# Performance work log

Measured on AMD Instinct MI355X. Metric: run time of the kernel, lower is better.

The kernel has to match this reference:

```python
import jax, jax.numpy as jnp
import numpy as np

B, F, V, D, K = 16384, 39, 30000, 16, 20
EPS = 1e-5


def bn_eval(x, g, b):
    # inference-mode BatchNorm1d with running_mean=0, running_var=1
    return g * x / jnp.sqrt(1.0 + EPS) + b


def setup_inputs() -> dict:
    key = jax.random.key(0)
    ks = jax.random.split(key, 12)
    x = jax.random.randint(ks[0], (B, F), 0, V)
    emb_table = jax.random.normal(ks[1], (F * V, D), dtype=jnp.float32) * 0.05
    w_c = jax.random.normal(ks[2], (F, F * D), dtype=jnp.float32) * 0.05
    w0 = jax.random.normal(ks[3], (1024, F * D), dtype=jnp.float32) * 0.04
    w1 = jax.random.normal(ks[4], (512, 1024), dtype=jnp.float32) * 0.03
    w_out = jax.random.normal(ks[5], (1, 512), dtype=jnp.float32) * 0.04
    return {
        'x': x, 'emb_table': emb_table,
        'w_c': w_c, 'b_c': jnp.zeros((F,)), 'g_c': jnp.ones((F,)), 'be_c': jnp.zeros((F,)),
        'w0': w0, 'b0': jnp.zeros((1024,)), 'g0': jnp.ones((1024,)), 'be0': jnp.zeros((1024,)),
        'w1': w1, 'b1': jnp.zeros((512,)), 'g1': jnp.ones((512,)), 'be1': jnp.zeros((512,)),
        'w_out': w_out, 'b_out': jnp.zeros((1,)),
    }


def reference(x, emb_table, w_c, b_c, g_c, be_c, w0, b0, g0, be0,
              w1, b1, g1, be1, w_out, b_out):
    offsets = jnp.arange(F, dtype=x.dtype) * V          # per-field offsets
    idx = x + offsets[None, :]                          # [B, F]
    emb = emb_table[idx]                                # [B, F, D] gather

    # controller_mlp: flatten (batch, D, F) layout like torch transpose(1,2)
    flat = jnp.transpose(emb, (0, 2, 1)).reshape(B, F * D)
    h = jax.nn.relu(bn_eval(flat @ w_c.T + b_c, g_c, be_c))
    scores = jax.nn.softmax(h, axis=1)                  # [B, F]

    # kmax_pooling: top-k field indices, sorted ascending, gather weights
    _, kidx = jax.lax.top_k(scores, K)
    kidx = jnp.sort(kidx, axis=1)                       # [B, K]
    w = jnp.take_along_axis(scores, kidx, axis=1)       # [B, K]

    # forward_select: gather selected field embeddings, weight them
    sel = jnp.take_along_axis(emb, kidx[:, :, None], axis=1)  # [B, K, D]
    weighted = sel * w[:, :, None]

    # scatter back into full field slots (unselected fields are zero)
    full = jnp.zeros((B, F, D), weighted.dtype)
    bidx = jnp.arange(B)[:, None]
    full = full.at[bidx, kidx].set(weighted)            # [B, F, D]

    z = jnp.transpose(full, (0, 2, 1)).reshape(B, F * D)
    z = jax.nn.relu(bn_eval(z @ w0.T + b0, g0, be0))
    z = jax.nn.relu(bn_eval(z @ w1.T + b1, g1, be1))
    out = jax.nn.sigmoid(z @ w_out.T + b_out)           # [B, 1]
    return out.squeeze(-1)
```

## Files before the change

### kernel.cpp

```cpp
#include <hip/hip_runtime.h>
#include <math.h>

#define B_SZ 16384
#define F_N 39
#define V_N 30000
#define D_N 16
#define K_SEL 20
#define FD 624
#define KP0 640
#define NCP 48
#define N0 1024
#define N1 512
#define CBR 16
#define ALD 648

typedef unsigned short u16;
typedef __attribute__((ext_vector_type(8))) short bf16x8;
typedef __attribute__((ext_vector_type(8))) unsigned short u16x8;
typedef __attribute__((ext_vector_type(4))) float f32x4;
typedef __attribute__((ext_vector_type(4))) unsigned short u16x4;

__device__ __forceinline__ u16 f2bf(float v) {
    union { float f; unsigned u; } x; x.f = v;
    unsigned r = x.u + 0x7fff + ((x.u >> 16) & 1);
    return (u16)(r >> 16);
}
__device__ __forceinline__ float bf2f(u16 v) {
    union { unsigned u; float f; } x; x.u = ((unsigned)v) << 16;
    return x.f;
}
__device__ __forceinline__ unsigned cvtpk2(float a, float b) {
    unsigned d;
    asm("v_cvt_pk_bf16_f32 %0, %1, %2" : "=v"(d) : "v"(a), "v"(b));
    return d;
}

#define GLD16(gp, lp) __builtin_amdgcn_global_load_lds( \
    (const __attribute__((address_space(1))) unsigned int*)(gp), \
    (__attribute__((address_space(3))) unsigned int*)(lp), 16, 0, 0)

__global__ __launch_bounds__(256) void prep_all_kernel(
    const float* __restrict__ w0, const float* __restrict__ w1,
    const float* __restrict__ w_c, const float* __restrict__ b_c,
    const float* __restrict__ g_c, const float* __restrict__ be_c,
    u16* __restrict__ w0b, u16* __restrict__ w1b, u16* __restrict__ wcb,
    float* __restrict__ bcp, float* __restrict__ gcp, float* __restrict__ becp,
    float* __restrict__ outp)
{
    __shared__ float Lb[8][624];
    const int bid = blockIdx.x;
    const int t   = threadIdx.x;

    if (bid < 134) {
        const bool is_w0 = (bid < 128);
        const int r0 = is_w0 ? bid * 8 : (bid - 128) * 8;
        const int nrows_src = is_w0 ? N0 : F_N;
        const float* __restrict__ src = is_w0 ? w0 : w_c;
        u16* __restrict__ dst = is_w0 ? w0b : wcb;

        for (int j = t; j < 8 * 156; j += 256) {
            const int row = j / 156;
            const int c4  = j - row * 156;
            const int n   = r0 + row;
            if (n < nrows_src)
                *(float4*)&Lb[row][c4 * 4] =
                    *(const float4*)&src[(size_t)n * FD + c4 * 4];
        }
        __syncthreads();

        for (int j = t; j < 8 * 320; j += 256) {
            const int row = j / 320;
            const int pr  = j - row * 320;
            const int n   = r0 + row;
            const int k0  = pr * 2;
            float v0 = 0.f, v1 = 0.f;
            if (n < nrows_src) {
                const int d0 = k0 & 15,       f0 = k0 >> 4;
                const int d1 = (k0 + 1) & 15, f1 = (k0 + 1) >> 4;
                if (f0 < F_N) v0 = Lb[row][d0 * F_N + f0];
                if (f1 < F_N) v1 = Lb[row][d1 * F_N + f1];
            }
            *(unsigned*)&dst[(size_t)n * KP0 + k0] = cvtpk2(v0, v1);
        }
        return;
    }
    if (bid < 390) {
        const size_t e0 = (size_t)(bid - 134) * 2048 + t * 8;
        float4 v0 = *(const float4*)(w1 + e0);
        float4 v1 = *(const float4*)(w1 + e0 + 4);
        uint4 o = { cvtpk2(v0.x, v0.y), cvtpk2(v0.z, v0.w),
                    cvtpk2(v1.x, v1.y), cvtpk2(v1.z, v1.w) };
        *(uint4*)(w1b + e0) = o;
        return;
    }
    if (bid < 398) {
        const size_t e0 = (size_t)(bid - 390) * 2048 + t * 8;
        float4 z = {0.f, 0.f, 0.f, 0.f};
        *(float4*)(outp + e0)     = z;
        *(float4*)(outp + e0 + 4) = z;
        return;
    }
    if (t < 3 * NCP) {
        const int which = t / NCP, n = t - which * NCP;
        float v = 0.f;
        if (n < F_N) v = (which == 0) ? b_c[n] : (which == 1) ? g_c[n] : be_c[n];
        ((which == 0) ? bcp : (which == 1) ? gcp : becp)[n] = v;
    }
}

__global__ __launch_bounds__(256) void fused_controller_kernel(
    const int* __restrict__ x, const float* __restrict__ emb_table,
    const u16* __restrict__ wcb, const float* __restrict__ bcp,
    const float* __restrict__ gcp, const float* __restrict__ becp,
    u16* __restrict__ zb)
{
    __shared__ __align__(16) u16 Al[CBR * ALD];
    __shared__ float vv[CBR][49];
    __shared__ f32x4 part[4][64][3];
    __shared__ float selw[CBR][F_N];

    const int t    = threadIdx.x;
    const int wave = t >> 6;
    const int lane = t & 63;
    const int b0   = blockIdx.x * CBR;

    {
        const int p0 = t, p1 = t + 256, p2 = t + 512;
        const int xi0 = x[b0 * F_N + p0];
        const int xi1 = x[b0 * F_N + p1];
        const int xi2 = (p2 < CBR * F_N) ? x[b0 * F_N + p2] : 0;
        const int pp[3] = { p0, p1, p2 };
        const int xx[3] = { xi0, xi1, xi2 };
        #pragma unroll
        for (int s = 0; s < 3; ++s) {
            const int p = pp[s];
            if (p < CBR * F_N) {
                const int row = p / F_N;
                const int f   = p - row * F_N;
                const float4* src =
                    (const float4*)(emb_table + (size_t)(xx[s] + f * V_N) * D_N);
                float4 v0 = src[0], v1 = src[1], v2 = src[2], v3 = src[3];
                uint4 o0 = { cvtpk2(v0.x, v0.y), cvtpk2(v0.z, v0.w),
                             cvtpk2(v1.x, v1.y), cvtpk2(v1.z, v1.w) };
                uint4 o1 = { cvtpk2(v2.x, v2.y), cvtpk2(v2.z, v2.w),
                             cvtpk2(v3.x, v3.y), cvtpk2(v3.z, v3.w) };
                *(uint4*)&Al[row * ALD + f * D_N]     = o0;
                *(uint4*)&Al[row * ALD + f * D_N + 8] = o1;
            }
        }
    }
    __syncthreads();

    const int m = lane & 15;
    const int q = lane >> 4;
    f32x4 acc0 = {}, acc1 = {}, acc2 = {};
    {
        const u16* ap  = &Al[m * ALD + wave * 160 + q * 8];
        const u16* bp0 = wcb + (size_t)(0  + m) * KP0 + wave * 160 + q * 8;
        const u16* bp1 = wcb + (size_t)(16 + m) * KP0 + wave * 160 + q * 8;
        const u16* bp2 = wcb + (size_t)(32 + m) * KP0 + wave * 160 + q * 8;
        #pragma unroll
        for (int k = 0; k < 5; ++k) {
            bf16x8 af = *(const bf16x8*)ap;
            bf16x8 b0 = *(const bf16x8*)bp0;
            bf16x8 b1 = *(const bf16x8*)bp1;
            bf16x8 b2 = *(const bf16x8*)bp2;
            acc0 = __builtin_amdgcn_mfma_f32_16x16x32_bf16(af, b0, acc0, 0, 0, 0);
            acc1 = __builtin_amdgcn_mfma_f32_16x16x32_bf16(af, b1, acc1, 0, 0, 0);
            acc2 = __builtin_amdgcn_mfma_f32_16x16x32_bf16(af, b2, acc2, 0, 0, 0);
            ap += 32; bp0 += 32; bp1 += 32; bp2 += 32;
        }
    }
    part[wave][lane][0] = acc0;
    part[wave][lane][1] = acc1;
    part[wave][lane][2] = acc2;
    __syncthreads();

    {
        f32x4 r0 = part[0][lane][0] + part[1][lane][0] + part[2][lane][0] + part[3][lane][0];
        f32x4 r1 = part[0][lane][1] + part[1][lane][1] + part[2][lane][1] + part[3][lane][1];
        f32x4 r2 = part[0][lane][2] + part[1][lane][2] + part[2][lane][2] + part[3][lane][2];

        const float rs = rsqrtf(1.0f + 1e-5f);
        if (q == wave) {
            #pragma unroll
            for (int j = 0; j < 3; ++j) {
                const f32x4 a = (j == 0) ? r0 : (j == 1) ? r1 : r2;
                const int n = j * 16 + m;
                const float gn = gcp[n] * rs;
                const float bn = becp[n];
                const float bi = bcp[n];
                #pragma unroll
                for (int r = 0; r < 4; ++r)
                    vv[wave * 4 + r][n] = fmaxf(fmaf(gn, a[r] + bi, bn), 0.f);
            }
        }
    }
    __syncthreads();

    {
        const int row = wave * 4 + (lane >> 4);
        const int fl  = lane & 15;
        float e[3] = {0.f, 0.f, 0.f};
        float mloc = -1e30f;
        #pragma unroll
        for (int it = 0; it < 3; ++it) {
            const int f = fl + 16 * it;
            if (f < F_N) { e[it] = vv[row][f]; mloc = fmaxf(mloc, e[it]); }
        }
        mloc = fmaxf(mloc, __shfl_xor(mloc, 1, 64));
        mloc = fmaxf(mloc, __shfl_xor(mloc, 2, 64));
        mloc = fmaxf(mloc, __shfl_xor(mloc, 4, 64));
        mloc = fmaxf(mloc, __shfl_xor(mloc, 8, 64));
        float sloc = 0.f;
        #pragma unroll
        for (int it = 0; it < 3; ++it) {
            const int f = fl + 16 * it;
            if (f < F_N) { e[it] = expf(e[it] - mloc); sloc += e[it]; }
        }
        sloc += __shfl_xor(sloc, 1, 64);
        sloc += __shfl_xor(sloc, 2, 64);
        sloc += __shfl_xor(sloc, 4, 64);
        sloc += __shfl_xor(sloc, 8, 64);
        const float inv = 1.f / sloc;
        #pragma unroll
        for (int it = 0; it < 3; ++it) {
            const int f = fl + 16 * it;
            if (f < F_N) vv[row][f] = e[it];
        }

        int rank[3] = {};
        for (int gg = 0; gg < F_N; ++gg) {
            const float o = vv[row][gg];
            #pragma unroll
            for (int it = 0; it < 3; ++it) {
                const int f = fl + 16 * it;
                if (f < F_N)
                    rank[it] += (o > e[it] || (o == e[it] && gg < f)) ? 1 : 0;
            }
        }
        #pragma unroll
        for (int it = 0; it < 3; ++it) {
            const int f = fl + 16 * it;
            if (f < F_N)
                selw[row][f] = (rank[it] < K_SEL) ? e[it] * inv : 0.f;
        }
    }
    __syncthreads();

    for (int gp = t; gp < CBR * 40; gp += 256) {
        const int row  = gp / 40;
        const int slot = gp - row * 40;
        u16* dst = zb + (size_t)(b0 + row) * KP0 + slot * D_N;
        uint4 o0 = {0u,0u,0u,0u}, o1 = {0u,0u,0u,0u};
        if (slot < F_N) {
            const float w = selw[row][slot];
            u16x8 a0 = *(u16x8*)&Al[row * ALD + slot * D_N];
            u16x8 a1 = *(u16x8*)&Al[row * ALD + slot * D_N + 8];
            o0 = (uint4){ cvtpk2(bf2f(a0[0]) * w, bf2f(a0[1]) * w),
                          cvtpk2(bf2f(a0[2]) * w, bf2f(a0[3]) * w),
                          cvtpk2(bf2f(a0[4]) * w, bf2f(a0[5]) * w),
                          cvtpk2(bf2f(a0[6]) * w, bf2f(a0[7]) * w) };
            o1 = (uint4){ cvtpk2(bf2f(a1[0]) * w, bf2f(a1[1]) * w),
                          cvtpk2(bf2f(a1[2]) * w, bf2f(a1[3]) * w),
                          cvtpk2(bf2f(a1[4]) * w, bf2f(a1[5]) * w),
                          cvtpk2(bf2f(a1[6]) * w, bf2f(a1[7]) * w) };
        }
        *(uint4*)dst       = o0;
        *(uint4*)(dst + 8) = o1;
    }
}

template<int MODE>
__global__ __launch_bounds__(512) void gemm_mfma_bn_relu(
    const u16* __restrict__ A, const u16* __restrict__ W,
    const float* __restrict__ bias, const float* __restrict__ g,
    const float* __restrict__ be, u16* __restrict__ Cout,
    int M, int N, int Kp,
    const float* __restrict__ w_out, float* __restrict__ outp)
{
    __shared__ __align__(16) u16 SM[3 * 12288];

    const int t    = threadIdx.x;
    const int wave = t >> 6;
    const int lane = t & 63;
    const int wm   = wave >> 1, wn = wave & 1;
    const int m0   = blockIdx.x * 256;
    const int n0   = blockIdx.y * 128;

    const int rA0 = t >> 2;
    const int cA0 = (t & 3) ^ ((rA0 >> 1) & 3);
    const int rA1 = 128 + rA0;
    const int cA1 = (t & 3) ^ ((rA1 >> 1) & 3);
    const u16* gA0 = A + (size_t)(m0 + rA0) * Kp + cA0 * 8;
    const u16* gA1 = A + (size_t)(m0 + rA1) * Kp + cA1 * 8;
    const u16* gB  = W + (size_t)(n0 + rA0) * Kp + cA0 * 8;
    const int dA0 = t * 8, dA1 = 4096 + t * 8, dB = 8192 + t * 8;

    const int q    = lane >> 4;
    const int lr16 = lane & 15;

    int aoff[4], boff[4];
    #pragma unroll
    for (int i = 0; i < 4; ++i) {
        int ra = wm * 64 + i * 16 + lr16;
        aoff[i] = ra * 32 + ((q ^ ((ra >> 1) & 3)) * 8);
        int rb = wn * 64 + i * 16 + lr16;
        boff[i] = rb * 32 + ((q ^ ((rb >> 1) & 3)) * 8);
    }

    const int NIT = Kp >> 5;

    GLD16(gA0, SM + dA0);
    GLD16(gA1, SM + dA1);
    GLD16(gB,  SM + dB);
    gA0 += 32; gA1 += 32; gB += 32;
    GLD16(gA0, SM + 12288 + dA0);
    GLD16(gA1, SM + 12288 + dA1);
    GLD16(gB,  SM + 12288 + dB);
    gA0 += 32; gA1 += 32; gB += 32;

    f32x4 acc[4][4] = {};
    int cur = 0, stg = 2;

    for (int it = 0; it < NIT - 1; ++it) {
        asm volatile("s_waitcnt vmcnt(3)" ::: "memory");
        __builtin_amdgcn_s_barrier();
        __builtin_amdgcn_sched_barrier(0);

        const u16* ac = SM + cur * 12288;
        const u16* bc = ac + 8192;

        bf16x8 af0 = *(const bf16x8*)(ac + aoff[0]);
        bf16x8 af1 = *(const bf16x8*)(ac + aoff[1]);
        bf16x8 b0v = *(const bf16x8*)(bc + boff[0]);
        bf16x8 b1v = *(const bf16x8*)(bc + boff[1]);
        bf16x8 b2v = *(const bf16x8*)(bc + boff[2]);
        bf16x8 b3v = *(const bf16x8*)(bc + boff[3]);

        if (it + 2 < NIT) {
            u16* s = SM + stg * 12288;
            GLD16(gA0, s + dA0);
            GLD16(gA1, s + dA1);
            GLD16(gB,  s + dB);
            gA0 += 32; gA1 += 32; gB += 32;
        }

        asm volatile("s_waitcnt lgkmcnt(0)" ::: "memory");
        __builtin_amdgcn_sched_barrier(0);
        __builtin_amdgcn_s_setprio(1);
        acc[0][0] = __builtin_amdgcn_mfma_f32_16x16x32_bf16(af0, b0v, acc[0][0], 0, 0, 0);
        acc[0][1] = __builtin_amdgcn_mfma_f32_16x16x32_bf16(af0, b1v, acc[0][1], 0, 0, 0);
        acc[0][2] = __builtin_amdgcn_mfma_f32_16x16x32_bf16(af0, b2v, acc[0][2], 0, 0, 0);
        acc[0][3] = __builtin_amdgcn_mfma_f32_16x16x32_bf16(af0, b3v, acc[0][3], 0, 0, 0);
        acc[1][0] = __builtin_amdgcn_mfma_f32_16x16x32_bf16(af1, b0v, acc[1][0], 0, 0, 0);
        acc[1][1] = __builtin_amdgcn_mfma_f32_16x16x32_bf16(af1, b1v, acc[1][1], 0, 0, 0);
        acc[1][2] = __builtin_amdgcn_mfma_f32_16x16x32_bf16(af1, b2v, acc[1][2], 0, 0, 0);
        acc[1][3] = __builtin_amdgcn_mfma_f32_16x16x32_bf16(af1, b3v, acc[1][3], 0, 0, 0);
        __builtin_amdgcn_s_setprio(0);
        __builtin_amdgcn_s_barrier();

        bf16x8 af2 = *(const bf16x8*)(ac + aoff[2]);
        bf16x8 af3 = *(const bf16x8*)(ac + aoff[3]);
        asm volatile("s_waitcnt lgkmcnt(0)" ::: "memory");
        __builtin_amdgcn_sched_barrier(0);
        __builtin_amdgcn_s_setprio(1);
        acc[2][0] = __builtin_amdgcn_mfma_f32_16x16x32_bf16(af2, b0v, acc[2][0], 0, 0, 0);
        acc[2][1] = __builtin_amdgcn_mfma_f32_16x16x32_bf16(af2, b1v, acc[2][1], 0, 0, 0);
        acc[2][2] = __builtin_amdgcn_mfma_f32_16x16x32_bf16(af2, b2v, acc[2][2], 0, 0, 0);
        acc[2][3] = __builtin_amdgcn_mfma_f32_16x16x32_bf16(af2, b3v, acc[2][3], 0, 0, 0);
        acc[3][0] = __builtin_amdgcn_mfma_f32_16x16x32_bf16(af3, b0v, acc[3][0], 0, 0, 0);
        acc[3][1] = __builtin_amdgcn_mfma_f32_16x16x32_bf16(af3, b1v, acc[3][1], 0, 0, 0);
        acc[3][2] = __builtin_amdgcn_mfma_f32_16x16x32_bf16(af3, b2v, acc[3][2], 0, 0, 0);
        acc[3][3] = __builtin_amdgcn_mfma_f32_16x16x32_bf16(af3, b3v, acc[3][3], 0, 0, 0);
        __builtin_amdgcn_s_setprio(0);

        cur = (cur == 2) ? 0 : cur + 1;
        stg = (stg == 2) ? 0 : stg + 1;
    }

    asm volatile("s_waitcnt vmcnt(0)" ::: "memory");
    __builtin_amdgcn_s_barrier();
    __builtin_amdgcn_sched_barrier(0);
    {
        const u16* ac = SM + cur * 12288;
        const u16* bc = ac + 8192;
        bf16x8 af[4], bfr[4];
        #pragma unroll
        for (int i = 0; i < 4; ++i) af[i]  = *(const bf16x8*)(ac + aoff[i]);
        #pragma unroll
        for (int j = 0; j < 4; ++j) bfr[j] = *(const bf16x8*)(bc + boff[j]);
        __builtin_amdgcn_s_setprio(1);
        #pragma unroll
        for (int i = 0; i < 4; ++i)
            #pragma unroll
            for (int j = 0; j < 4; ++j)
                acc[i][j] = __builtin_amdgcn_mfma_f32_16x16x32_bf16(
                    af[i], bfr[j], acc[i][j], 0, 0, 0);
        __builtin_amdgcn_s_setprio(0);
    }

    const float rs = rsqrtf(1.0f + 1e-5f);
    if (MODE == 0) {
        __syncthreads();
        u16* Cs = SM;
        #pragma unroll
        for (int j = 0; j < 4; ++j) {
            const int nl = wn * 64 + j * 16 + lr16;
            const int n  = n0 + nl;
            const float bn_g = g[n] * rs;
            const float bn_b = be[n];
            const float bi   = bias[n];
            #pragma unroll
            for (int i = 0; i < 4; ++i) {
                const int mlb = wm * 64 + i * 16 + q * 4;
                float v0 = fmaxf(fmaf(bn_g, acc[i][j][0] + bi, bn_b), 0.f);
                float v1 = fmaxf(fmaf(bn_g, acc[i][j][1] + bi, bn_b), 0.f);
                float v2 = fmaxf(fmaf(bn_g, acc[i][j][2] + bi, bn_b), 0.f);
                float v3 = fmaxf(fmaf(bn_g, acc[i][j][3] + bi, bn_b), 0.f);
                unsigned pA = cvtpk2(v0, v1);
                unsigned pB = cvtpk2(v2, v3);
                Cs[(mlb + 0) * 136 + nl] = (u16)pA;
                Cs[(mlb + 1) * 136 + nl] = (u16)(pA >> 16);
                Cs[(mlb + 2) * 136 + nl] = (u16)pB;
                Cs[(mlb + 3) * 136 + nl] = (u16)(pB >> 16);
            }
        }
        __syncthreads();
        #pragma unroll
        for (int s = 0; s < 8; ++s) {
            const int chunk = s * 512 + t;
            const int row   = chunk >> 4;
            const int col   = (chunk & 15) << 3;
            *(u16x8*)&Cout[(size_t)(m0 + row) * N + n0 + col] =
                *(const u16x8*)&Cs[row * 136 + col];
        }
    } else {
        float s[4][4] = {};
        #pragma unroll
        for (int j = 0; j < 4; ++j) {
            const int n = n0 + wn * 64 + j * 16 + lr16;
            const float bn_g = g[n] * rs;
            const float bn_b = be[n];
            const float bi   = bias[n];
            const float wo   = w_out[n];
            #pragma unroll
            for (int i = 0; i < 4; ++i)
                #pragma unroll
                for (int r = 0; r < 4; ++r) {
                    float v = acc[i][j][r] + bi;
                    v = fmaxf(fmaf(bn_g, v, bn_b), 0.f);
                    s[i][r] = fmaf(v, wo, s[i][r]);
                }
        }
        #pragma unroll
        for (int i = 0; i < 4; ++i)
            #pragma unroll
            for (int r = 0; r < 4; ++r) {
                float v = s[i][r];
                v += __shfl_xor(v, 1, 64);
                v += __shfl_xor(v, 2, 64);
                v += __shfl_xor(v, 4, 64);
                v += __shfl_xor(v, 8, 64);
                s[i][r] = v;
            }
        if (lr16 == 0) {
            #pragma unroll
            for (int i = 0; i < 4; ++i) {
                const int mbase = m0 + wm * 64 + i * 16 + q * 4;
                #pragma unroll
                for (int r = 0; r < 4; ++r)
                    atomicAdd(&outp[mbase + r], s[i][r]);
            }
        }
    }
}

__global__ __launch_bounds__(256) void sigmoid_kernel(
    const float* __restrict__ outp, const float* __restrict__ b_out,
    float* __restrict__ out)
{
    const int b = blockIdx.x * 256 + threadIdx.x;
    out[b] = 1.f / (1.f + expf(-(outp[b] + b_out[0])));
}

extern "C" void kernel_launch(void* const* d_in, const int* in_sizes, int n_in,
                              void* d_out, int out_size, void* d_ws, size_t ws_size,
                              hipStream_t stream)
{
    const int*   x     = (const int*)  d_in[0];
    const float* emb   = (const float*)d_in[1];
    const float* w_c   = (const float*)d_in[2];
    const float* b_c   = (const float*)d_in[3];
    const float* g_c   = (const float*)d_in[4];
    const float* be_c  = (const float*)d_in[5];
    const float* w0    = (const float*)d_in[6];
    const float* b0    = (const float*)d_in[7];
    const float* g0    = (const float*)d_in[8];
    const float* be0   = (const float*)d_in[9];
    const float* w1    = (const float*)d_in[10];
    const float* b1    = (const float*)d_in[11];
    const float* g1    = (const float*)d_in[12];
    const float* be1   = (const float*)d_in[13];
    const float* w_out = (const float*)d_in[14];
    const float* b_out = (const float*)d_in[15];
    float* out = (float*)d_out;

    u16*   zb    = (u16*)d_ws;
    u16*   w0b   = zb    + (size_t)B_SZ * KP0;
    u16*   h0b   = w0b   + (size_t)N0 * KP0;
    u16*   w1b   = h0b   + (size_t)B_SZ * N0;
    u16*   wcb   = w1b   + (size_t)N1 * N0;
    float* outp  = (float*)(wcb + (size_t)NCP * KP0);
    float* bcp   = outp + B_SZ;
    float* gcp   = bcp + NCP;
    float* becp  = gcp + NCP;

    prep_all_kernel<<<399, 256, 0, stream>>>(
        w0, w1, w_c, b_c, g_c, be_c, w0b, w1b, wcb, bcp, gcp, becp, outp);

    fused_controller_kernel<<<B_SZ / CBR, 256, 0, stream>>>(
        x, emb, wcb, bcp, gcp, becp, zb);

    gemm_mfma_bn_relu<0><<<dim3(B_SZ / 256, N0 / 128), 512, 0, stream>>>(
        zb, w0b, b0, g0, be0, h0b, B_SZ, N0, KP0, nullptr, nullptr);

    gemm_mfma_bn_relu<1><<<dim3(B_SZ / 256, N1 / 128), 512, 0, stream>>>(
        h0b, w1b, b1, g1, be1, nullptr, B_SZ, N1, N0, w_out, outp);

    sigmoid_kernel<<<B_SZ / 256, 256, 0, stream>>>(outp, b_out, out);
}
```

Measured before the change: 205.6 us.

## Fuse both MLP GEMMs, output projection and sigmoid into one kernel

```diff
diff --git a/kernel.cpp b/kernel.cpp
--- a/kernel.cpp
+++ b/kernel.cpp
@@ -18,13 +18,7 @@
 typedef __attribute__((ext_vector_type(8))) short bf16x8;
 typedef __attribute__((ext_vector_type(8))) unsigned short u16x8;
 typedef __attribute__((ext_vector_type(4))) float f32x4;
-typedef __attribute__((ext_vector_type(4))) unsigned short u16x4;
-
-__device__ __forceinline__ u16 f2bf(float v) {
-    union { float f; unsigned u; } x; x.f = v;
-    unsigned r = x.u + 0x7fff + ((x.u >> 16) & 1);
-    return (u16)(r >> 16);
-}
+
 __device__ __forceinline__ float bf2f(u16 v) {
     union { unsigned u; float f; } x; x.u = ((unsigned)v) << 16;
     return x.f;
@@ -39,13 +33,14 @@
     (const __attribute__((address_space(1))) unsigned int*)(gp), \
     (__attribute__((address_space(3))) unsigned int*)(lp), 16, 0, 0)
 
+#define MFMA16(a, b, c) __builtin_amdgcn_mfma_f32_16x16x32_bf16((a), (b), (c), 0, 0, 0)
+
 __global__ __launch_bounds__(256) void prep_all_kernel(
     const float* __restrict__ w0, const float* __restrict__ w1,
     const float* __restrict__ w_c, const float* __restrict__ b_c,
     const float* __restrict__ g_c, const float* __restrict__ be_c,
     u16* __restrict__ w0b, u16* __restrict__ w1b, u16* __restrict__ wcb,
-    float* __restrict__ bcp, float* __restrict__ gcp, float* __restrict__ becp,
-    float* __restrict__ outp)
+    float* __restrict__ bcp, float* __restrict__ gcp, float* __restrict__ becp)
 {
     __shared__ float Lb[8][624];
     const int bid = blockIdx.x;
@@ -91,13 +86,6 @@
         uint4 o = { cvtpk2(v0.x, v0.y), cvtpk2(v0.z, v0.w),
                     cvtpk2(v1.x, v1.y), cvtpk2(v1.z, v1.w) };
         *(uint4*)(w1b + e0) = o;
-        return;
-    }
-    if (bid < 398) {
-        const size_t e0 = (size_t)(bid - 390) * 2048 + t * 8;
-        float4 z = {0.f, 0.f, 0.f, 0.f};
-        *(float4*)(outp + e0)     = z;
-        *(float4*)(outp + e0 + 4) = z;
         return;
     }
     if (t < 3 * NCP) {
@@ -162,12 +150,12 @@
         #pragma unroll
         for (int k = 0; k < 5; ++k) {
             bf16x8 af = *(const bf16x8*)ap;
-            bf16x8 b0 = *(const bf16x8*)bp0;
-            bf16x8 b1 = *(const bf16x8*)bp1;
-            bf16x8 b2 = *(const bf16x8*)bp2;
-            acc0 = __builtin_amdgcn_mfma_f32_16x16x32_bf16(af, b0, acc0, 0, 0, 0);
-            acc1 = __builtin_amdgcn_mfma_f32_16x16x32_bf16(af, b1, acc1, 0, 0, 0);
-            acc2 = __builtin_amdgcn_mfma_f32_16x16x32_bf16(af, b2, acc2, 0, 0, 0);
+            bf16x8 b0r = *(const bf16x8*)bp0;
+            bf16x8 b1r = *(const bf16x8*)bp1;
+            bf16x8 b2r = *(const bf16x8*)bp2;
+            acc0 = MFMA16(af, b0r, acc0);
+            acc1 = MFMA16(af, b1r, acc1);
+            acc2 = MFMA16(af, b2r, acc2);
             ap += 32; bp0 += 32; bp1 += 32; bp2 += 32;
         }
     }
@@ -271,217 +259,294 @@
     }
 }
 
-template<int MODE>
-__global__ __launch_bounds__(512) void gemm_mfma_bn_relu(
-    const u16* __restrict__ A, const u16* __restrict__ W,
-    const float* __restrict__ bias, const float* __restrict__ g,
-    const float* __restrict__ be, u16* __restrict__ Cout,
-    int M, int N, int Kp,
-    const float* __restrict__ w_out, float* __restrict__ outp)
+__global__ __launch_bounds__(512) void fused_mlp_kernel(
+    const u16* __restrict__ Azb, const u16* __restrict__ W0,
+    const u16* __restrict__ W1,
+    const float* __restrict__ b0v, const float* __restrict__ g0v,
+    const float* __restrict__ be0v,
+    const float* __restrict__ b1v, const float* __restrict__ g1v,
+    const float* __restrict__ be1v,
+    const float* __restrict__ wov, const float* __restrict__ bov,
+    float* __restrict__ out)
 {
-    __shared__ __align__(16) u16 SM[3 * 12288];
+    __shared__ __align__(16) u16 SM[3 * 16384];
+    __shared__ __align__(16) u16 H0[64 * 264];
+    __shared__ float red[4][64];
 
     const int t    = threadIdx.x;
+    const int lane = t & 63;
     const int wave = t >> 6;
-    const int lane = t & 63;
-    const int wm   = wave >> 1, wn = wave & 1;
-    const int m0   = blockIdx.x * 256;
-    const int n0   = blockIdx.y * 128;
-
-    const int rA0 = t >> 2;
-    const int cA0 = (t & 3) ^ ((rA0 >> 1) & 3);
-    const int rA1 = 128 + rA0;
-    const int cA1 = (t & 3) ^ ((rA1 >> 1) & 3);
-    const u16* gA0 = A + (size_t)(m0 + rA0) * Kp + cA0 * 8;
-    const u16* gA1 = A + (size_t)(m0 + rA1) * Kp + cA1 * 8;
-    const u16* gB  = W + (size_t)(n0 + rA0) * Kp + cA0 * 8;
-    const int dA0 = t * 8, dA1 = 4096 + t * 8, dB = 8192 + t * 8;
-
-    const int q    = lane >> 4;
-    const int lr16 = lane & 15;
-
-    int aoff[4], boff[4];
+    const int wm = wave >> 2, wn = wave & 3;
+    const int q = lane >> 4, lr16 = lane & 15;
+    const int brow = blockIdx.x * 64;
+
+    const int srow = t >> 2;
+    const int cC   = (t & 3) ^ ((t >> 3) & 3);
+    const int dA  = t * 8;
+    const int dB0 = 2048 + t * 8;
+    const int dB1 = 2048 + (t + 512) * 8;
+
+    const u16* gAz = Azb + (size_t)(brow + srow) * KP0 + cC * 8;
+
+    int aoffA[2], boffA[4], aoffB[2], boffB[8];
     #pragma unroll
-    for (int i = 0; i < 4; ++i) {
-        int ra = wm * 64 + i * 16 + lr16;
-        aoff[i] = ra * 32 + ((q ^ ((ra >> 1) & 3)) * 8);
-        int rb = wn * 64 + i * 16 + lr16;
-        boff[i] = rb * 32 + ((q ^ ((rb >> 1) & 3)) * 8);
-    }
-
-    const int NIT = Kp >> 5;
-
-    GLD16(gA0, SM + dA0);
-    GLD16(gA1, SM + dA1);
-    GLD16(gB,  SM + dB);
-    gA0 += 32; gA1 += 32; gB += 32;
-    GLD16(gA0, SM + 12288 + dA0);
-    GLD16(gA1, SM + 12288 + dA1);
-    GLD16(gB,  SM + 12288 + dB);
-    gA0 += 32; gA1 += 32; gB += 32;
-
-    f32x4 acc[4][4] = {};
-    int cur = 0, stg = 2;
-
-    for (int it = 0; it < NIT - 1; ++it) {
-        asm volatile("s_waitcnt vmcnt(3)" ::: "memory");
+    for (int i = 0; i < 2; ++i) {
+        const int ra = wm * 32 + i * 16 + lr16;
+        aoffA[i] = ra * 32 + ((q ^ ((ra >> 1) & 3)) * 8);
+        aoffB[i] = ra * 264 + q * 8;
+    }
+    #pragma unroll
+    for (int j = 0; j < 4; ++j) {
+        const int rb = wn * 64 + j * 16 + lr16;
+        boffA[j] = 2048 + rb * 32 + ((q ^ ((rb >> 1) & 3)) * 8);
+    }
+    #pragma unroll
+    for (int j = 0; j < 8; ++j) {
+        const int rb = wn * 128 + j * 16 + lr16;
+        boffB[j] = rb * 32 + ((q ^ ((rb >> 1) & 3)) * 8);
+    }
+
+    f32x4 acc1[2][8] = {};
+    const float rs = rsqrtf(1.0f + 1e-5f);
+
+    for (int nt = 0; nt < 4; ++nt) {
+        f32x4 acc0[2][4] = {};
+        const u16* pA  = gAz;
+        const u16* pB0 = W0 + (size_t)(nt * 256 + srow)       * KP0 + cC * 8;
+        const u16* pB1 = W0 + (size_t)(nt * 256 + srow + 128) * KP0 + cC * 8;
+
+        if (t < 256) GLD16(pA, SM + dA);
+        GLD16(pB0, SM + dB0);
+        GLD16(pB1, SM + dB1);
+        pA += 32; pB0 += 32; pB1 += 32;
+        if (t < 256) GLD16(pA, SM + 16384 + dA);
+        GLD16(pB0, SM + 16384 + dB0);
+        GLD16(pB1, SM + 16384 + dB1);
+        pA += 32; pB0 += 32; pB1 += 32;
+
+        int cur = 0, stg = 2;
+        for (int it = 0; it < 19; ++it) {
+            if (t < 256) { asm volatile("s_waitcnt vmcnt(3)" ::: "memory"); }
+            else         { asm volatile("s_waitcnt vmcnt(2)" ::: "memory"); }
+            __builtin_amdgcn_s_barrier();
+            __builtin_amdgcn_sched_barrier(0);
+            const u16* sc = SM + cur * 16384;
+            bf16x8 a0 = *(const bf16x8*)(sc + aoffA[0]);
+            bf16x8 a1 = *(const bf16x8*)(sc + aoffA[1]);
+            bf16x8 f0 = *(const bf16x8*)(sc + boffA[0]);
+            bf16x8 f1 = *(const bf16x8*)(sc + boffA[1]);
+            bf16x8 f2 = *(const bf16x8*)(sc + boffA[2]);
+            bf16x8 f3 = *(const bf16x8*)(sc + boffA[3]);
+            if (it + 2 < 20) {
+                u16* ss = SM + stg * 16384;
+                if (t < 256) GLD16(pA, ss + dA);
+                GLD16(pB0, ss + dB0);
+                GLD16(pB1, ss + dB1);
+                pA += 32; pB0 += 32; pB1 += 32;
+            }
+            asm volatile("s_waitcnt lgkmcnt(0)" ::: "memory");
+            __builtin_amdgcn_sched_barrier(0);
+            __builtin_amdgcn_s_setprio(1);
+            acc0[0][0] = MFMA16(a0, f0, acc0[0][0]);
+            acc0[0][1] = MFMA16(a0, f1, acc0[0][1]);
+            acc0[0][2] = MFMA16(a0, f2, acc0[0][2]);
+            acc0[0][3] = MFMA16(a0, f3, acc0[0][3]);
+            acc0[1][0] = MFMA16(a1, f0, acc0[1][0]);
+            acc0[1][1] = MFMA16(a1, f1, acc0[1][1]);
+            acc0[1][2] = MFMA16(a1, f2, acc0[1][2]);
+            acc0[1][3] = MFMA16(a1, f3, acc0[1][3]);
+            __builtin_amdgcn_s_setprio(0);
+            cur = (cur == 2) ? 0 : cur + 1;
+            stg = (stg == 2) ? 0 : stg + 1;
+        }
+        asm volatile("s_waitcnt vmcnt(0)" ::: "memory");
         __builtin_amdgcn_s_barrier();
         __builtin_amdgcn_sched_barrier(0);
-
-        const u16* ac = SM + cur * 12288;
-        const u16* bc = ac + 8192;
-
-        bf16x8 af0 = *(const bf16x8*)(ac + aoff[0]);
-        bf16x8 af1 = *(const bf16x8*)(ac + aoff[1]);
-        bf16x8 b0v = *(const bf16x8*)(bc + boff[0]);
-        bf16x8 b1v = *(const bf16x8*)(bc + boff[1]);
-        bf16x8 b2v = *(const bf16x8*)(bc + boff[2]);
-        bf16x8 b3v = *(const bf16x8*)(bc + boff[3]);
-
-        if (it + 2 < NIT) {
-            u16* s = SM + stg * 12288;
-            GLD16(gA0, s + dA0);
-            GLD16(gA1, s + dA1);
-            GLD16(gB,  s + dB);
-            gA0 += 32; gA1 += 32; gB += 32;
-        }
-
+        {
+            const u16* sc = SM + 16384;
+            bf16x8 a0 = *(const bf16x8*)(sc + aoffA[0]);
+            bf16x8 a1 = *(const bf16x8*)(sc + aoffA[1]);
+            bf16x8 f0 = *(const bf16x8*)(sc + boffA[0]);
+            bf16x8 f1 = *(const bf16x8*)(sc + boffA[1]);
+            bf16x8 f2 = *(const bf16x8*)(sc + boffA[2]);
+            bf16x8 f3 = *(const bf16x8*)(sc + boffA[3]);
+            asm volatile("s_waitcnt lgkmcnt(0)" ::: "memory");
+            __builtin_amdgcn_sched_barrier(0);
+            __builtin_amdgcn_s_setprio(1);
+            acc0[0][0] = MFMA16(a0, f0, acc0[0][0]);
+            acc0[0][1] = MFMA16(a0, f1, acc0[0][1]);
+            acc0[0][2] = MFMA16(a0, f2, acc0[0][2]);
+            acc0[0][3] = MFMA16(a0, f3, acc0[0][3]);
+            acc0[1][0] = MFMA16(a1, f0, acc0[1][0]);
+            acc0[1][1] = MFMA16(a1, f1, acc0[1][1]);
+            acc0[1][2] = MFMA16(a1, f2, acc0[1][2]);
+            acc0[1][3] = MFMA16(a1, f3, acc0[1][3]);
+            __builtin_amdgcn_s_setprio(0);
+        }
+
+        const u16* pC = W1 + (size_t)srow * N0 + nt * 256 + cC * 8;
+        {
+            GLD16(pC,               SM + t * 8);
+            GLD16(pC + 131072,      SM + (t + 512) * 8);
+            GLD16(pC + 262144,      SM + (t + 1024) * 8);
+            GLD16(pC + 393216,      SM + (t + 1536) * 8);
+            u16* s2 = SM + 2 * 16384;
+            GLD16(pC + 32,          s2 + t * 8);
+            GLD16(pC + 131072 + 32, s2 + (t + 512) * 8);
+            GLD16(pC + 262144 + 32, s2 + (t + 1024) * 8);
+            GLD16(pC + 393216 + 32, s2 + (t + 1536) * 8);
+        }
+
+        #pragma unroll
+        for (int j = 0; j < 4; ++j) {
+            const int n = nt * 256 + wn * 64 + j * 16 + lr16;
+            const float gg = g0v[n] * rs;
+            const float bb = be0v[n];
+            const float bi = b0v[n];
+            const int colL = wn * 64 + j * 16 + lr16;
+            #pragma unroll
+            for (int i = 0; i < 2; ++i) {
+                const int mlb = wm * 32 + i * 16 + q * 4;
+                float v0 = fmaxf(fmaf(gg, acc0[i][j][0] + bi, bb), 0.f);
+                float v1 = fmaxf(fmaf(gg, acc0[i][j][1] + bi, bb), 0.f);
+                float v2 = fmaxf(fmaf(gg, acc0[i][j][2] + bi, bb), 0.f);
+                float v3 = fmaxf(fmaf(gg, acc0[i][j][3] + bi, bb), 0.f);
+                unsigned pa = cvtpk2(v0, v1);
+                unsigned pb = cvtpk2(v2, v3);
+                H0[(mlb + 0) * 264 + colL] = (u16)pa;
+                H0[(mlb + 1) * 264 + colL] = (u16)(pa >> 16);
+                H0[(mlb + 2) * 264 + colL] = (u16)pb;
+                H0[(mlb + 3) * 264 + colL] = (u16)(pb >> 16);
+            }
+        }
         asm volatile("s_waitcnt lgkmcnt(0)" ::: "memory");
+        __builtin_amdgcn_s_barrier();
+
+        const u16* pCk = pC + 64;
+        int cb = 0, sb = 1;
+        for (int ks = 0; ks < 7; ++ks) {
+            asm volatile("s_waitcnt vmcnt(4)" ::: "memory");
+            __builtin_amdgcn_s_barrier();
+            __builtin_amdgcn_sched_barrier(0);
+            const u16* sc = SM + cb * 16384;
+            bf16x8 a0 = *(const bf16x8*)(&H0[aoffB[0] + ks * 32]);
+            bf16x8 a1 = *(const bf16x8*)(&H0[aoffB[1] + ks * 32]);
+            bf16x8 f0 = *(const bf16x8*)(sc + boffB[0]);
+            bf16x8 f1 = *(const bf16x8*)(sc + boffB[1]);
+            bf16x8 f2 = *(const bf16x8*)(sc + boffB[2]);
+            bf16x8 f3 = *(const bf16x8*)(sc + boffB[3]);
+            bf16x8 f4 = *(const bf16x8*)(sc + boffB[4]);
+            bf16x8 f5 = *(const bf16x8*)(sc + boffB[5]);
+            bf16x8 f6 = *(const bf16x8*)(sc + boffB[6]);
+            bf16x8 f7 = *(const bf16x8*)(sc + boffB[7]);
+            if (ks + 2 < 8) {
+                u16* ss = SM + sb * 16384;
+                GLD16(pCk,          ss + t * 8);
+                GLD16(pCk + 131072, ss + (t + 512) * 8);
+                GLD16(pCk + 262144, ss + (t + 1024) * 8);
+                GLD16(pCk + 393216, ss + (t + 1536) * 8);
+                pCk += 32;
+            }
+            asm volatile("s_waitcnt lgkmcnt(0)" ::: "memory");
+            __builtin_amdgcn_sched_barrier(0);
+            __builtin_amdgcn_s_setprio(1);
+            acc1[0][0] = MFMA16(a0, f0, acc1[0][0]);
+            acc1[0][1] = MFMA16(a0, f1, acc1[0][1]);
+            acc1[0][2] = MFMA16(a0, f2, acc1[0][2]);
+            acc1[0][3] = MFMA16(a0, f3, acc1[0][3]);
+            acc1[0][4] = MFMA16(a0, f4, acc1[0][4]);
+            acc1[0][5] = MFMA16(a0, f5, acc1[0][5]);
+            acc1[0][6] = MFMA16(a0, f6, acc1[0][6]);
+            acc1[0][7] = MFMA16(a0, f7, acc1[0][7]);
+            acc1[1][0] = MFMA16(a1, f0, acc1[1][0]);
+            acc1[1][1] = MFMA16(a1, f1, acc1[1][1]);
+            acc1[1][2] = MFMA16(a1, f2, acc1[1][2]);
+            acc1[1][3] = MFMA16(a1, f3, acc1[1][3]);
+            acc1[1][4] = MFMA16(a1, f4, acc1[1][4]);
+            acc1[1][5] = MFMA16(a1, f5, acc1[1][5]);
+            acc1[1][6] = MFMA16(a1, f6, acc1[1][6]);
+            acc1[1][7] = MFMA16(a1, f7, acc1[1][7]);
+            __builtin_amdgcn_s_setprio(0);
+            cb = (cb == 0) ? 2 : cb - 1;
+            sb = (sb == 0) ? 2 : sb - 1;
+        }
+        asm volatile("s_waitcnt vmcnt(0)" ::: "memory");
+        __builtin_amdgcn_s_barrier();
         __builtin_amdgcn_sched_barrier(0);
-        __builtin_amdgcn_s_setprio(1);
-        acc[0][0] = __builtin_amdgcn_mfma_f32_16x16x32_bf16(af0, b0v, acc[0][0], 0, 0, 0);
-        acc[0][1] = __builtin_amdgcn_mfma_f32_16x16x32_bf16(af0, b1v, acc[0][1], 0, 0, 0);
-        acc[0][2] = __builtin_amdgcn_mfma_f32_16x16x32_bf16(af0, b2v, acc[0][2], 0, 0, 0);
-        acc[0][3] = __builtin_amdgcn_mfma_f32_16x16x32_bf16(af0, b3v, acc[0][3], 0, 0, 0);
-        acc[1][0] = __builtin_amdgcn_mfma_f32_16x16x32_bf16(af1, b0v, acc[1][0], 0, 0, 0);
-        acc[1][1] = __builtin_amdgcn_mfma_f32_16x16x32_bf16(af1, b1v, acc[1][1], 0, 0, 0);
-        acc[1][2] = __builtin_amdgcn_mfma_f32_16x16x32_bf16(af1, b2v, acc[1][2], 0, 0, 0);
-        acc[1][3] = __builtin_amdgcn_mfma_f32_16x16x32_bf16(af1, b3v, acc[1][3], 0, 0, 0);
-        __builtin_amdgcn_s_setprio(0);
-        __builtin_amdgcn_s_barrier();
-
-        bf16x8 af2 = *(const bf16x8*)(ac + aoff[2]);
-        bf16x8 af3 = *(const bf16x8*)(ac + aoff[3]);
-        asm volatile("s_waitcnt lgkmcnt(0)" ::: "memory");
-        __builtin_amdgcn_sched_barrier(0);
-        __builtin_amdgcn_s_setprio(1);
-        acc[2][0] = __builtin_amdgcn_mfma_f32_16x16x32_bf16(af2, b0v, acc[2][0], 0, 0, 0);
-        acc[2][1] = __builtin_amdgcn_mfma_f32_16x16x32_bf16(af2, b1v, acc[2][1], 0, 0, 0);
-        acc[2][2] = __builtin_amdgcn_mfma_f32_16x16x32_bf16(af2, b2v, acc[2][2], 0, 0, 0);
-        acc[2][3] = __builtin_amdgcn_mfma_f32_16x16x32_bf16(af2, b3v, acc[2][3], 0, 0, 0);
-        acc[3][0] = __builtin_amdgcn_mfma_f32_16x16x32_bf16(af3, b0v, acc[3][0], 0, 0, 0);
-        acc[3][1] = __builtin_amdgcn_mfma_f32_16x16x32_bf16(af3, b1v, acc[3][1], 0, 0, 0);
-        acc[3][2] = __builtin_amdgcn_mfma_f32_16x16x32_bf16(af3, b2v, acc[3][2], 0, 0, 0);
-        acc[3][3] = __builtin_amdgcn_mfma_f32_16x16x32_bf16(af3, b3v, acc[3][3], 0, 0, 0);
-        __builtin_amdgcn_s_setprio(0);
-
-        cur = (cur == 2) ? 0 : cur + 1;
-        stg = (stg == 2) ? 0 : stg + 1;
-    }
-
-    asm volatile("s_waitcnt vmcnt(0)" ::: "memory");
-    __builtin_amdgcn_s_barrier();
-    __builtin_amdgcn_sched_barrier(0);
-    {
-        const u16* ac = SM + cur * 12288;
-        const u16* bc = ac + 8192;
-        bf16x8 af[4], bfr[4];
-        #pragma unroll
-        for (int i = 0; i < 4; ++i) af[i]  = *(const bf16x8*)(ac + aoff[i]);
-        #pragma unroll
-        for (int j = 0; j < 4; ++j) bfr[j] = *(const bf16x8*)(bc + boff[j]);
-        __builtin_amdgcn_s_setprio(1);
-        #pragma unroll
-        for (int i = 0; i < 4; ++i)
-            #pragma unroll
-            for (int j = 0; j < 4; ++j)
-                acc[i][j] = __builtin_amdgcn_mfma_f32_16x16x32_bf16(
-                    af[i], bfr[j], acc[i][j], 0, 0, 0);
-        __builtin_amdgcn_s_setprio(0);
-    }
-
-    const float rs = rsqrtf(1.0f + 1e-5f);
-    if (MODE == 0) {
-        __syncthreads();
-        u16* Cs = SM;
-        #pragma unroll
-        for (int j = 0; j < 4; ++j) {
-            const int nl = wn * 64 + j * 16 + lr16;
-            const int n  = n0 + nl;
-            const float bn_g = g[n] * rs;
-            const float bn_b = be[n];
-            const float bi   = bias[n];
-            #pragma unroll
-            for (int i = 0; i < 4; ++i) {
-                const int mlb = wm * 64 + i * 16 + q * 4;
-                float v0 = fmaxf(fmaf(bn_g, acc[i][j][0] + bi, bn_b), 0.f);
-                float v1 = fmaxf(fmaf(bn_g, acc[i][j][1] + bi, bn_b), 0.f);
-                float v2 = fmaxf(fmaf(bn_g, acc[i][j][2] + bi, bn_b), 0.f);
-                float v3 = fmaxf(fmaf(bn_g, acc[i][j][3] + bi, bn_b), 0.f);
-                unsigned pA = cvtpk2(v0, v1);
-                unsigned pB = cvtpk2(v2, v3);
-                Cs[(mlb + 0) * 136 + nl] = (u16)pA;
-                Cs[(mlb + 1) * 136 + nl] = (u16)(pA >> 16);
-                Cs[(mlb + 2) * 136 + nl] = (u16)pB;
-                Cs[(mlb + 3) * 136 + nl] = (u16)(pB >> 16);
-            }
-        }
-        __syncthreads();
-        #pragma unroll
-        for (int s = 0; s < 8; ++s) {
-            const int chunk = s * 512 + t;
-            const int row   = chunk >> 4;
-            const int col   = (chunk & 15) << 3;
-            *(u16x8*)&Cout[(size_t)(m0 + row) * N + n0 + col] =
-                *(const u16x8*)&Cs[row * 136 + col];
-        }
-    } else {
-        float s[4][4] = {};
-        #pragma unroll
-        for (int j = 0; j < 4; ++j) {
-            const int n = n0 + wn * 64 + j * 16 + lr16;
-            const float bn_g = g[n] * rs;
-            const float bn_b = be[n];
-            const float bi   = bias[n];
-            const float wo   = w_out[n];
-            #pragma unroll
-            for (int i = 0; i < 4; ++i)
-                #pragma unroll
-                for (int r = 0; r < 4; ++r) {
-                    float v = acc[i][j][r] + bi;
-                    v = fmaxf(fmaf(bn_g, v, bn_b), 0.f);
-                    s[i][r] = fmaf(v, wo, s[i][r]);
-                }
-        }
-        #pragma unroll
-        for (int i = 0; i < 4; ++i)
+        {
+            const u16* sc = SM + 2 * 16384;
+            bf16x8 a0 = *(const bf16x8*)(&H0[aoffB[0] + 7 * 32]);
+            bf16x8 a1 = *(const bf16x8*)(&H0[aoffB[1] + 7 * 32]);
+            bf16x8 f0 = *(const bf16x8*)(sc + boffB[0]);
+            bf16x8 f1 = *(const bf16x8*)(sc + boffB[1]);
+            bf16x8 f2 = *(const bf16x8*)(sc + boffB[2]);
+            bf16x8 f3 = *(const bf16x8*)(sc + boffB[3]);
+            bf16x8 f4 = *(const bf16x8*)(sc + boffB[4]);
+            bf16x8 f5 = *(const bf16x8*)(sc + boffB[5]);
+            bf16x8 f6 = *(const bf16x8*)(sc + boffB[6]);
+            bf16x8 f7 = *(const bf16x8*)(sc + boffB[7]);
+            asm volatile("s_waitcnt lgkmcnt(0)" ::: "memory");
+            __builtin_amdgcn_sched_barrier(0);
+            __builtin_amdgcn_s_setprio(1);
+            acc1[0][0] = MFMA16(a0, f0, acc1[0][0]);
+            acc1[0][1] = MFMA16(a0, f1, acc1[0][1]);
+            acc1[0][2] = MFMA16(a0, f2, acc1[0][2]);
+            acc1[0][3] = MFMA16(a0, f3, acc1[0][3]);
+            acc1[0][4] = MFMA16(a0, f4, acc1[0][4]);
+            acc1[0][5] = MFMA16(a0, f5, acc1[0][5]);
+            acc1[0][6] = MFMA16(a0, f6, acc1[0][6]);
+            acc1[0][7] = MFMA16(a0, f7, acc1[0][7]);
+            acc1[1][0] = MFMA16(a1, f0, acc1[1][0]);
+            acc1[1][1] = MFMA16(a1, f1, acc1[1][1]);
+            acc1[1][2] = MFMA16(a1, f2, acc1[1][2]);
+            acc1[1][3] = MFMA16(a1, f3, acc1[1][3]);
+            acc1[1][4] = MFMA16(a1, f4, acc1[1][4]);
+            acc1[1][5] = MFMA16(a1, f5, acc1[1][5]);
+            acc1[1][6] = MFMA16(a1, f6, acc1[1][6]);
+            acc1[1][7] = MFMA16(a1, f7, acc1[1][7]);
+            __builtin_amdgcn_s_setprio(0);
+        }
+    }
+
+    float s[2][4] = {};
+    #pragma unroll
+    for (int j = 0; j < 8; ++j) {
+        const int n1 = wn * 128 + j * 16 + lr16;
+        const float wv = wov[n1];
+        const float gg = g1v[n1] * rs;
+        const float bb = be1v[n1];
+        const float bi = b1v[n1];
+        #pragma unroll
+        for (int i = 0; i < 2; ++i)
             #pragma unroll
             for (int r = 0; r < 4; ++r) {
-                float v = s[i][r];
-                v += __shfl_xor(v, 1, 64);
-                v += __shfl_xor(v, 2, 64);
-                v += __shfl_xor(v, 4, 64);
-                v += __shfl_xor(v, 8, 64);
-                s[i][r] = v;
-            }
-        if (lr16 == 0) {
+                float v = fmaxf(fmaf(gg, acc1[i][j][r] + bi, bb), 0.f);
+                s[i][r] = fmaf(v, wv, s[i][r]);
+            }
+    }
+    #pragma unroll
+    for (int i = 0; i < 2; ++i)
+        #pragma unroll
+        for (int r = 0; r < 4; ++r) {
+            float v = s[i][r];
+            v += __shfl_xor(v, 1, 64);
+            v += __shfl_xor(v, 2, 64);
+            v += __shfl_xor(v, 4, 64);
+            v += __shfl_xor(v, 8, 64);
+            s[i][r] = v;
+        }
+    if (lr16 == 0) {
+        #pragma unroll
+        for (int i = 0; i < 2; ++i)
             #pragma unroll
-            for (int i = 0; i < 4; ++i) {
-                const int mbase = m0 + wm * 64 + i * 16 + q * 4;
-                #pragma unroll
-                for (int r = 0; r < 4; ++r)
-                    atomicAdd(&outp[mbase + r], s[i][r]);
-            }
-        }
-    }
-}
-
-__global__ __launch_bounds__(256) void sigmoid_kernel(
-    const float* __restrict__ outp, const float* __restrict__ b_out,
-    float* __restrict__ out)
-{
-    const int b = blockIdx.x * 256 + threadIdx.x;
-    out[b] = 1.f / (1.f + expf(-(outp[b] + b_out[0])));
+            for (int r = 0; r < 4; ++r)
+                red[wn][wm * 32 + i * 16 + q * 4 + r] = s[i][r];
+    }
+    __syncthreads();
+    if (t < 64) {
+        const float v = red[0][t] + red[1][t] + red[2][t] + red[3][t] + bov[0];
+        out[brow + t] = 1.f / (1.f + expf(-v));
+    }
 }
 
 extern "C" void kernel_launch(void* const* d_in, const int* in_sizes, int n_in,
@@ -507,26 +572,19 @@
     float* out = (float*)d_out;
 
     u16*   zb    = (u16*)d_ws;
-    u16*   w0b   = zb    + (size_t)B_SZ * KP0;
-    u16*   h0b   = w0b   + (size_t)N0 * KP0;
-    u16*   w1b   = h0b   + (size_t)B_SZ * N0;
-    u16*   wcb   = w1b   + (size_t)N1 * N0;
-    float* outp  = (float*)(wcb + (size_t)NCP * KP0);
-    float* bcp   = outp + B_SZ;
+    u16*   w0b   = zb  + (size_t)B_SZ * KP0;
+    u16*   w1b   = w0b + (size_t)N0 * KP0;
+    u16*   wcb   = w1b + (size_t)N1 * N0;
+    float* bcp   = (float*)(wcb + (size_t)NCP * KP0);
     float* gcp   = bcp + NCP;
     float* becp  = gcp + NCP;
 
-    prep_all_kernel<<<399, 256, 0, stream>>>(
-        w0, w1, w_c, b_c, g_c, be_c, w0b, w1b, wcb, bcp, gcp, becp, outp);
+    prep_all_kernel<<<391, 256, 0, stream>>>(
+        w0, w1, w_c, b_c, g_c, be_c, w0b, w1b, wcb, bcp, gcp, becp);
 
     fused_controller_kernel<<<B_SZ / CBR, 256, 0, stream>>>(
         x, emb, wcb, bcp, gcp, becp, zb);
 
-    gemm_mfma_bn_relu<0><<<dim3(B_SZ / 256, N0 / 128), 512, 0, stream>>>(
-        zb, w0b, b0, g0, be0, h0b, B_SZ, N0, KP0, nullptr, nullptr);
-
-    gemm_mfma_bn_relu<1><<<dim3(B_SZ / 256, N1 / 128), 512, 0, stream>>>(
-        h0b, w1b, b1, g1, be1, nullptr, B_SZ, N1, N0, w_out, outp);
-
-    sigmoid_kernel<<<B_SZ / 256, 256, 0, stream>>>(outp, b_out, out);
+    fused_mlp_kernel<<<B_SZ / 64, 512, 0, stream>>>(
+        zb, w0b, w1b, b0, g0, be0, b1, g1, be1, w_out, b_out, out);
 }
```

After: 221.8 us. 1.08x slower.
